# Kernel tuning notes

Hardware: AMD Instinct MI355X
Metric: run time of the kernel (lower is better)

Reference implementation:

```python
import jax, jax.numpy as jnp
import numpy as np

B, L, E, H, Dff = 2, 2048, 1024, 16, 4096
Dh = E // H


def _ln(x, g, b, eps=1e-5):
    m = jnp.mean(x, axis=-1, keepdims=True)
    v = jnp.mean((x - m) ** 2, axis=-1, keepdims=True)
    return (x - m) / jnp.sqrt(v + eps) * g + b


def setup_inputs() -> dict:
    key = jax.random.key(0)
    ks = jax.random.split(key, 16)
    s_e = 1.0 / np.sqrt(E)
    s_d = 1.0 / np.sqrt(Dff)
    inp = {
        "x": jax.random.normal(ks[0], (B, L, E), jnp.float32),
        # causal mask: positions with 0 are masked out (masked_fill(mask==0, -1e9))
        "mask": jnp.tril(jnp.ones((L, L), jnp.bool_)),
        # per-head QKV projections, stacked over heads: (H, E, Dh), biases (H, Dh)
        "Wq": jax.random.uniform(ks[1], (H, E, Dh), jnp.float32, -s_e, s_e),
        "bq": jax.random.uniform(ks[2], (H, Dh), jnp.float32, -s_e, s_e),
        "Wk": jax.random.uniform(ks[3], (H, E, Dh), jnp.float32, -s_e, s_e),
        "bk": jax.random.uniform(ks[4], (H, Dh), jnp.float32, -s_e, s_e),
        "Wv": jax.random.uniform(ks[5], (H, E, Dh), jnp.float32, -s_e, s_e),
        "bv": jax.random.uniform(ks[6], (H, Dh), jnp.float32, -s_e, s_e),
        "Wo": jax.random.uniform(ks[7], (E, E), jnp.float32, -s_e, s_e),
        "bo": jax.random.uniform(ks[8], (E,), jnp.float32, -s_e, s_e),
        "W1": jax.random.uniform(ks[9], (E, Dff), jnp.float32, -s_e, s_e),
        "c1": jax.random.uniform(ks[10], (Dff,), jnp.float32, -s_e, s_e),
        "W2": jax.random.uniform(ks[11], (Dff, E), jnp.float32, -s_d, s_d),
        "c2": jax.random.uniform(ks[12], (E,), jnp.float32, -s_d, s_d),
        "g1": jnp.ones((E,), jnp.float32),
        "beta1": jnp.zeros((E,), jnp.float32),
        "g2": jnp.ones((E,), jnp.float32),
        "beta2": jnp.zeros((E,), jnp.float32),
    }
    return inp


def reference(x, mask, Wq, bq, Wk, bk, Wv, bv, Wo, bo, W1, c1, W2, c2, g1, beta1, g2, beta2):
    # Batched equivalent of the per-head Attention loop (eval mode: dropout = identity)
    q = jnp.einsum("ble,hed->bhld", x, Wq) + bq[None, :, None, :]
    k = jnp.einsum("ble,hed->bhld", x, Wk) + bk[None, :, None, :]
    v = jnp.einsum("ble,hed->bhld", x, Wv) + bv[None, :, None, :]
    scores = jnp.einsum("bhld,bhmd->bhlm", q, k) / np.sqrt(Dh).astype(np.float32)
    scores = jnp.where(mask[None, None, :, :], scores, -1e9)
    p = jax.nn.softmax(scores, axis=-1)
    z = jnp.einsum("bhlm,bhmd->bhld", p, v)  # (B,H,L,Dh)
    z = z.transpose(0, 2, 1, 3).reshape(B, L, E)  # concat heads
    att = z @ Wo + bo
    h = _ln(x + att, g1, beta1)
    ff = jax.nn.relu(h @ W1 + c1) @ W2 + c2
    out = _ln(h + ff, g2, beta2)
    return out
```

## Files before the change

kernel.cpp:

```cpp
#include <hip/hip_runtime.h>
#include <hip/hip_bf16.h>
#include <math.h>

#define B_   2
#define L_   2048
#define E_   1024
#define H_   16
#define DH   64
#define DFF  4096
#define M_   4096
#define APAD 72
#define SCALE_Q 0.18033688011112042f

typedef __attribute__((ext_vector_type(8))) short short8;
typedef __attribute__((ext_vector_type(4))) float f32x4;
typedef __bf16 bf16x8 __attribute__((ext_vector_type(8)));

__device__ __forceinline__ float bf2f(unsigned short u) {
    return __uint_as_float(((unsigned)u) << 16);
}
__device__ __forceinline__ unsigned short f2bf(float f) {
    unsigned u = __float_as_uint(f);
    return (unsigned short)((u + 0x7fff + ((u >> 16) & 1)) >> 16);
}
__device__ __forceinline__ unsigned pk_trunc(float lo, float hi) {
    return (__float_as_uint(lo) >> 16) | (__float_as_uint(hi) & 0xffff0000u);
}

__device__ __forceinline__ void gld16(const unsigned short* g, unsigned short* l) {
    __builtin_amdgcn_global_load_lds(
        (const __attribute__((address_space(1))) void*)g,
        (__attribute__((address_space(3))) void*)l, 16, 0, 0);
}

__global__ __launch_bounds__(256) void prep(const float* __restrict__ x,
                                            const float* __restrict__ Wq,
                                            const float* __restrict__ Wk,
                                            const float* __restrict__ Wv,
                                            const float* __restrict__ bq,
                                            const float* __restrict__ bk,
                                            const float* __restrict__ bv,
                                            const float* __restrict__ Wo,
                                            const float* __restrict__ W1,
                                            const float* __restrict__ W2,
                                            unsigned short* __restrict__ xb,
                                            unsigned short* __restrict__ Wqkvt,
                                            unsigned short* __restrict__ Wot,
                                            unsigned short* __restrict__ W1t,
                                            unsigned short* __restrict__ W2t,
                                            float* __restrict__ bqkv) {
    __shared__ float tile[32][33];
    int bid = blockIdx.x;
    const int t = threadIdx.x;

    if (bid < 4096) {
        int i = (bid * 256 + t) * 4;
        float4 v = *(const float4*)&x[i];
        ushort4 pk = { f2bf(v.x), f2bf(v.y), f2bf(v.z), f2bf(v.w) };
        *(ushort4*)&xb[i] = pk;
        return;
    }
    bid -= 4096;

    const float* in; unsigned short* outp; int R, C, r0, c0; float sc = 1.f;
    if (bid < 3072) {
        int xq = bid & 1, yq = (bid >> 1) & 31, wh = bid >> 6;
        int which = wh >> 4, h = wh & 15;
        in   = (which == 0 ? Wq : which == 1 ? Wk : Wv) + (size_t)h * E_ * DH;
        outp = Wqkvt + ((size_t)which * 1024 + h * 64) * 1024;
        R = E_; C = DH; r0 = yq * 32; c0 = xq * 32;
        if (which == 0) sc = SCALE_Q;
    } else if (bid < 4096) {
        bid -= 3072;
        in = Wo; outp = Wot; R = E_; C = E_;
        c0 = (bid & 31) * 32; r0 = (bid >> 5) * 32;
    } else if (bid < 8192) {
        bid -= 4096;
        in = W1; outp = W1t; R = E_; C = DFF;
        c0 = (bid & 127) * 32; r0 = (bid >> 7) * 32;
    } else if (bid < 12288) {
        bid -= 8192;
        in = W2; outp = W2t; R = DFF; C = E_;
        c0 = (bid & 31) * 32; r0 = (bid >> 5) * 32;
    } else {
        bid -= 12288;
        int n = bid * 256 + t;
        bqkv[n] = n < 1024 ? bq[n] * SCALE_Q : n < 2048 ? bk[n - 1024] : bv[n - 2048];
        return;
    }

    const int tx = t & 31, tq = t >> 5;
#pragma unroll
    for (int s2 = 0; s2 < 4; s2++)
        tile[tq * 4 + s2][tx] = in[(size_t)(r0 + tq * 4 + s2) * C + c0 + tx] * sc;
    __syncthreads();
#pragma unroll
    for (int s2 = 0; s2 < 4; s2++)
        outp[(size_t)(c0 + tq * 4 + s2) * R + r0 + tx] = f2bf(tile[tx][tq * 4 + s2]);
}

__global__ __launch_bounds__(256) void v_transpose_perm(const unsigned short* __restrict__ qkv,
                                                        unsigned short* __restrict__ vtg) {
    __shared__ unsigned short tile[64 * APAD];
    const int t  = threadIdx.x;
    const int kt = blockIdx.x, hh = blockIdx.y, b = blockIdx.z;
    const int rr0 = t >> 3, o8 = (t & 7) * 8, rr1 = rr0 + 32;
    const size_t gbase = ((size_t)b * L_ + kt * 64) * 3072 + 2048 + hh * 64;
    *(short8*)&tile[rr0 * APAD + o8] = *(const short8*)&qkv[gbase + (size_t)rr0 * 3072 + o8];
    *(short8*)&tile[rr1 * APAD + o8] = *(const short8*)&qkv[gbase + (size_t)rr1 * 3072 + o8];
    __syncthreads();
    const size_t obase = ((size_t)(b * H_ + hh) * 64) * (size_t)L_ + kt * 64;
    const int a = t & 15, d0 = (t >> 4) * 4;
#pragma unroll
    for (int s2 = 0; s2 < 4; s2++) {
        int d = d0 + s2;
        ushort4 pk = { tile[(a +  0) * APAD + d], tile[(a + 16) * APAD + d],
                       tile[(a + 32) * APAD + d], tile[(a + 48) * APAD + d] };
        *(ushort4*)&vtg[obase + (size_t)d * L_ + 4 * a] = pk;
    }
}

#define BAR() __builtin_amdgcn_s_barrier()
#define LGKM0() do { asm volatile("s_waitcnt lgkmcnt(0)" ::: "memory"); \
                     __builtin_amdgcn_sched_barrier(0); } while (0)

#define G256_READ_A(qr) do {                                                  \
    _Pragma("unroll") for (int mi = 0; mi < 4; mi++)                          \
    _Pragma("unroll") for (int ks = 0; ks < 2; ks++)                          \
        afr[mi][ks] = *(const bf16x8*)&As[bb + ((qr) * 128 + aRow + mi * 16) * 64 + (ks ? cs1 : cs0)]; \
} while (0)

#define G256_READ_B(qc) do {                                                  \
    _Pragma("unroll") for (int nj = 0; nj < 2; nj++)                          \
    _Pragma("unroll") for (int ks = 0; ks < 2; ks++)                          \
        bfr[qc][nj][ks] = *(const bf16x8*)&Bs[bb + ((qc) * 128 + bRow + nj * 16) * 64 + (ks ? cs1 : cs0)]; \
} while (0)

#define G256_MFMA(qr, qc) do {                                                \
    __builtin_amdgcn_s_setprio(1);                                            \
    _Pragma("unroll") for (int mi = 0; mi < 4; mi++)                          \
    _Pragma("unroll") for (int nj = 0; nj < 2; nj++)                          \
    _Pragma("unroll") for (int ks = 0; ks < 2; ks++)                          \
        acc[qr][qc][mi][nj] = __builtin_amdgcn_mfma_f32_16x16x32_bf16(        \
            afr[mi][ks], bfr[qc][nj][ks], acc[qr][qc][mi][nj], 0, 0, 0);      \
    __builtin_amdgcn_s_setprio(0);                                            \
} while (0)

template <int RELU, int SK>
__global__ __launch_bounds__(512, 2) void gemm256(const unsigned short* __restrict__ A,
                                                  const unsigned short* __restrict__ Bt,
                                                  const float* __restrict__ bias,
                                                  unsigned short* __restrict__ P0,
                                                  unsigned short* __restrict__ P1,
                                                  unsigned short* __restrict__ P2,
                                                  unsigned short* __restrict__ P3,
                                                  int M, int N, int K) {
    extern __shared__ __align__(16) unsigned short g_lds[];
    unsigned short* As = g_lds;
    unsigned short* Bs = g_lds + 32768;

    const int t    = threadIdx.x;
    const int lane = t & 63;
    const int w    = t >> 6;
    const int quad = lane >> 4;
    const int l16  = lane & 15;

    const int lin = blockIdx.x;
    const int xcd = lin & 7, s = lin >> 3;
    int m0, n0, kbeg, KT;
    unsigned short* C;
    if (SK) {
        m0 = ((xcd << 1) | (s & 1)) * 256;
        const int rest = s >> 1;
        n0 = (rest & 3) * 256;
        const int z  = rest >> 2;
        const int K4 = K >> 2;
        kbeg = z * K4;
        KT   = K4 >> 6;
        C = (z == 0) ? P0 : (z == 1) ? P1 : (z == 2) ? P2 : P3;
    } else {
        const int NT2 = (N >> 8) >> 1;
        m0 = (((xcd & 3) << 2) | (s & 3)) * 256;
        n0 = ((xcd >> 2) * NT2 + (s >> 2)) * 256;
        kbeg = 0;
        KT   = K >> 6;
        C = P0;
    }

    const int srow = t >> 3;
    const int ksw  = ((t & 7) ^ (srow & 7)) * 8;
    const size_t aStage = (size_t)(m0 + srow) * K + kbeg + ksw;
    const size_t bStage = (size_t)(n0 + srow) * K + kbeg + ksw;

    auto stageA = [&](int buf, int h, int v) {
        size_t g = aStage + (size_t)(h * 128) * K + (size_t)v * 64;
        unsigned short* l = As + buf * 16384 + h * 8192 + w * 512;
        gld16(A + g, l);
        gld16(A + g + (size_t)64 * K, l + 4096);
    };
    auto stageB = [&](int buf, int h, int v) {
        size_t g = bStage + (size_t)(h * 128) * K + (size_t)v * 64;
        unsigned short* l = Bs + buf * 16384 + h * 8192 + w * 512;
        gld16(Bt + g, l);
        gld16(Bt + g + (size_t)64 * K, l + 4096);
    };

    const int aRow = (w >> 2) * 64 + l16;
    const int bRow = (w & 3) * 32 + l16;
    const int cs0  = (quad ^ (l16 & 7)) * 8;
    const int cs1  = cs0 ^ 32;

    f32x4 acc[2][2][4][2];
#pragma unroll
    for (int a1 = 0; a1 < 2; a1++)
#pragma unroll
        for (int a2 = 0; a2 < 2; a2++)
#pragma unroll
            for (int a3 = 0; a3 < 4; a3++)
#pragma unroll
                for (int a4 = 0; a4 < 2; a4++)
                    acc[a1][a2][a3][a4] = (f32x4){0.f, 0.f, 0.f, 0.f};

    bf16x8 afr[4][2], bfr[2][2][2];

    stageA(0, 0, 0); stageA(0, 1, 0); stageB(0, 0, 0); stageB(0, 1, 0);
    if (KT > 1) {
        stageA(1, 0, 1); stageB(1, 0, 1);
        asm volatile("s_waitcnt vmcnt(4)" ::: "memory");
    } else {
        asm volatile("s_waitcnt vmcnt(0)" ::: "memory");
    }
    BAR();

    for (int u = 0; u < KT; ++u) {
        const int bb = (u & 1) * 16384;
        const int nb = ((u + 1) & 1);

        G256_READ_A(0);
        G256_READ_B(0);
        if (u + 1 < KT) stageB(nb, 1, u + 1);
        BAR(); LGKM0();
        G256_MFMA(0, 0);
        BAR();

        G256_READ_B(1);
        if (u + 1 < KT) stageA(nb, 1, u + 1);
        BAR(); LGKM0();
        G256_MFMA(0, 1);
        BAR();

        G256_READ_A(1);
        if (u + 2 < KT) stageA(u & 1, 0, u + 2);
        BAR(); LGKM0();
        G256_MFMA(1, 0);
        BAR();

        if (u + 2 < KT) {
            stageB(u & 1, 0, u + 2);
            asm volatile("s_waitcnt vmcnt(4)" ::: "memory");
        } else {
            asm volatile("s_waitcnt vmcnt(0)" ::: "memory");
        }
        BAR(); LGKM0();
        G256_MFMA(1, 1);
        BAR();
    }

#pragma unroll
    for (int qr = 0; qr < 2; qr++)
#pragma unroll
        for (int qc = 0; qc < 2; qc++)
#pragma unroll
            for (int nj = 0; nj < 2; nj++) {
                const int col = n0 + qc * 128 + (w & 3) * 32 + nj * 16 + l16;
                const float bv = SK ? 0.f : bias[col];
#pragma unroll
                for (int mi = 0; mi < 4; mi++) {
                    const int row = m0 + qr * 128 + (w >> 2) * 64 + mi * 16 + quad * 4;
#pragma unroll
                    for (int r = 0; r < 4; r++) {
                        float v = acc[qr][qc][mi][nj][r] + bv;
                        if (RELU) v = fmaxf(v, 0.f);
                        C[(size_t)(row + r) * N + col] = f2bf(v);
                    }
                }
            }
}

__global__ __launch_bounds__(256, 2) void attn_mfma(const unsigned short* __restrict__ qkv,
                                                    const unsigned short* __restrict__ vtg,
                                                    unsigned short* __restrict__ oA,
                                                    unsigned short* __restrict__ oB,
                                                    float* __restrict__ lA,
                                                    float* __restrict__ lB) {
    __shared__ __align__(16) unsigned short ks[2][64 * APAD];
    __shared__ __align__(16) unsigned short vt[64 * APAD];
    __shared__ __align__(16) unsigned short ps[128 * APAD];

    const int t    = threadIdx.x;
    const int lane = t & 63;
    const int w    = t >> 6;
    const int l16  = lane & 15;
    const int quad = lane >> 4;

    const int lin  = blockIdx.x;
    const int unit = lin >> 8;
    const int l8   = lin & 255;
    const int xcd  = l8 & 7;
    const int s    = l8 >> 3;
    const int hh   = xcd * 2 + (s & 1);
    const int rest = s >> 1;
    const int b    = rest & 1;
    const int pair = rest >> 1;

    unsigned short* __restrict__ oP = unit ? oB : oA;
    float* __restrict__ lP = unit ? lB : lA;

    const size_t rowbase = (size_t)b * L_;
    const size_t vbase   = ((size_t)(b * H_ + hh) * 64) * (size_t)L_;
    const int rr0 = t >> 3, o8 = (t & 7) * 8, rr1 = rr0 + 32;

    for (int ph = 0; ph < 2; ph++) {
        const int qq = ph ? pair : 15 - pair;
        const int cnt = qq + 1;

        bf16x8 qf[2][2];
#pragma unroll
        for (int g = 0; g < 2; g++) {
            size_t qrow = rowbase + qq * 128 + w * 32 + g * 16 + l16;
#pragma unroll
            for (int c = 0; c < 2; c++)
                qf[g][c] = *(const bf16x8*)&qkv[qrow * 3072 + hh * 64 + c * 32 + quad * 8];
        }

        f32x4 o[2][4];
#pragma unroll
        for (int g = 0; g < 2; g++)
#pragma unroll
            for (int j = 0; j < 4; j++) o[g][j] = (f32x4){0.f, 0.f, 0.f, 0.f};
        float l_i[2][4] = {};

        {
            size_t kg = (rowbase + unit * 64) * 3072 + 1024 + hh * 64;
            short8 k0 = *(const short8*)&qkv[kg + (size_t)rr0 * 3072 + o8];
            short8 k1 = *(const short8*)&qkv[kg + (size_t)rr1 * 3072 + o8];
            short8 v0 = *(const short8*)&vtg[vbase + unit * 64 + (size_t)rr0 * L_ + o8];
            short8 v1 = *(const short8*)&vtg[vbase + unit * 64 + (size_t)rr1 * L_ + o8];
            *(short8*)&ks[0][rr0 * APAD + o8] = k0;
            *(short8*)&ks[0][rr1 * APAD + o8] = k1;
            *(short8*)&vt[rr0 * APAD + o8] = v0;
            *(short8*)&vt[rr1 * APAD + o8] = v1;
        }

        short8 kr0, kr1, vr0, vr1;
        for (int i = 0; i < cnt; i++) {
            const int kt = unit + 2 * i;
            const int p  = i & 1;
            __syncthreads();

            if (i + 1 < cnt) {
                size_t kg = (rowbase + (kt + 2) * 64) * 3072 + 1024 + hh * 64;
                kr0 = *(const short8*)&qkv[kg + (size_t)rr0 * 3072 + o8];
                kr1 = *(const short8*)&qkv[kg + (size_t)rr1 * 3072 + o8];
                size_t vg = vbase + (kt + 2) * 64;
                vr0 = *(const short8*)&vtg[vg + (size_t)rr0 * L_ + o8];
                vr1 = *(const short8*)&vtg[vg + (size_t)rr1 * L_ + o8];
            }

            f32x4 s4[2][4];
#pragma unroll
            for (int g = 0; g < 2; g++)
#pragma unroll
                for (int j = 0; j < 4; j++) s4[g][j] = (f32x4){0.f, 0.f, 0.f, 0.f};
            __builtin_amdgcn_s_setprio(1);
#pragma unroll
            for (int c = 0; c < 2; c++)
#pragma unroll
                for (int j = 0; j < 4; j++) {
                    bf16x8 kf = *(const bf16x8*)&ks[p][(j * 16 + l16) * APAD + c * 32 + quad * 8];
#pragma unroll
                    for (int g = 0; g < 2; g++)
                        s4[g][j] = __builtin_amdgcn_mfma_f32_16x16x32_bf16(qf[g][c], kf, s4[g][j], 0, 0, 0);
                }
            __builtin_amdgcn_s_setprio(0);

            if (kt >= 2 * qq) {
#pragma unroll
                for (int g = 0; g < 2; g++)
#pragma unroll
                    for (int j = 0; j < 4; j++) {
                        int lk = kt * 64 + j * 16 + l16;
#pragma unroll
                        for (int r = 0; r < 4; r++)
                            if (lk > qq * 128 + w * 32 + g * 16 + quad * 4 + r)
                                s4[g][j][r] = -INFINITY;
                    }
            }

#pragma unroll
            for (int g = 0; g < 2; g++)
#pragma unroll
                for (int r = 0; r < 4; r++) {
                    float p0 = __builtin_amdgcn_exp2f(s4[g][0][r]);
                    float p1 = __builtin_amdgcn_exp2f(s4[g][1][r]);
                    float p2 = __builtin_amdgcn_exp2f(s4[g][2][r]);
                    float p3 = __builtin_amdgcn_exp2f(s4[g][3][r]);
                    l_i[g][r] += (p0 + p1) + (p2 + p3);
                    uint2 pk = { pk_trunc(p0, p1), pk_trunc(p2, p3) };
                    *(uint2*)&ps[(w * 32 + g * 16 + quad * 4 + r) * APAD + 4 * l16] = pk;
                }

            __builtin_amdgcn_s_waitcnt(0xc07f);

            __builtin_amdgcn_s_setprio(1);
#pragma unroll
            for (int c = 0; c < 2; c++) {
                bf16x8 pf[2];
#pragma unroll
                for (int g = 0; g < 2; g++)
                    pf[g] = *(const bf16x8*)&ps[(w * 32 + g * 16 + l16) * APAD + c * 32 + quad * 8];
#pragma unroll
                for (int j = 0; j < 4; j++) {
                    bf16x8 vf = *(const bf16x8*)&vt[(j * 16 + l16) * APAD + c * 32 + quad * 8];
#pragma unroll
                    for (int g = 0; g < 2; g++)
                        o[g][j] = __builtin_amdgcn_mfma_f32_16x16x32_bf16(pf[g], vf, o[g][j], 0, 0, 0);
                }
            }
            __builtin_amdgcn_s_setprio(0);

            __syncthreads();
            if (i + 1 < cnt) {
                *(short8*)&ks[p ^ 1][rr0 * APAD + o8] = kr0;
                *(short8*)&ks[p ^ 1][rr1 * APAD + o8] = kr1;
                *(short8*)&vt[rr0 * APAD + o8] = vr0;
                *(short8*)&vt[rr1 * APAD + o8] = vr1;
            }
        }

#pragma unroll
        for (int g = 0; g < 2; g++)
#pragma unroll
            for (int r = 0; r < 4; r++) {
                float l = l_i[g][r];
                l += __shfl_xor(l, 1);
                l += __shfl_xor(l, 2);
                l += __shfl_xor(l, 4);
                l += __shfl_xor(l, 8);
                int rowq = qq * 128 + w * 32 + g * 16 + quad * 4 + r;
                size_t grow = (size_t)(b * H_ + hh) * L_ + rowq;
                if (l16 == 0) lP[grow] = l;
#pragma unroll
                for (int j = 0; j < 4; j++)
                    oP[grow * 64 + j * 16 + l16] = f2bf(o[g][j][r]);
            }
    }
}

__global__ __launch_bounds__(256) void attn_combine(const unsigned short* __restrict__ oA,
                                                    const unsigned short* __restrict__ oB,
                                                    const float* __restrict__ lA,
                                                    const float* __restrict__ lB,
                                                    unsigned short* __restrict__ zb) {
    const int t = threadIdx.x;
    const size_t idx4 = ((size_t)blockIdx.x * 256 + t) * 4;
    const size_t row  = idx4 >> 6;
    const int    col  = (int)(idx4 & 63);

    float inv = 1.f / (lA[row] + lB[row]);
    ushort4 ua = *(const ushort4*)&oA[idx4];
    ushort4 ub = *(const ushort4*)&oB[idx4];

    const int bq   = (int)(row >> 15);
    const int hh   = (int)((row >> 11) & 15);
    const int rowq = (int)(row & 2047);
    size_t z = ((size_t)(bq * L_ + rowq)) * 1024 + hh * 64 + col;
    ushort4 pk = { f2bf((bf2f(ua.x) + bf2f(ub.x)) * inv),
                   f2bf((bf2f(ua.y) + bf2f(ub.y)) * inv),
                   f2bf((bf2f(ua.z) + bf2f(ub.z)) * inv),
                   f2bf((bf2f(ua.w) + bf2f(ub.w)) * inv) };
    *(ushort4*)&zb[z] = pk;
}

template <int WRITE_BF16>
__global__ __launch_bounds__(256) void ln5_kernel(const float* __restrict__ a,
                                                  const unsigned short* __restrict__ q0,
                                                  const unsigned short* __restrict__ q1,
                                                  const unsigned short* __restrict__ q2,
                                                  const unsigned short* __restrict__ q3,
                                                  const float* __restrict__ bias,
                                                  const float* __restrict__ g,
                                                  const float* __restrict__ be,
                                                  float* __restrict__ out,
                                                  unsigned short* __restrict__ out_bf) {
    __shared__ float s1[256], s2[256];
    const int row = blockIdx.x;
    const int t   = threadIdx.x;
    const size_t base = (size_t)row * E_ + t * 4;

    float4 ya = *(const float4*)&a[base];
    ushort4 u0 = *(const ushort4*)&q0[base];
    ushort4 u1 = *(const ushort4*)&q1[base];
    ushort4 u2 = *(const ushort4*)&q2[base];
    ushort4 u3 = *(const ushort4*)&q3[base];
    float4 bb = *(const float4*)&bias[t * 4];
    float y0 = ya.x + bb.x + bf2f(u0.x) + bf2f(u1.x) + bf2f(u2.x) + bf2f(u3.x);
    float y1 = ya.y + bb.y + bf2f(u0.y) + bf2f(u1.y) + bf2f(u2.y) + bf2f(u3.y);
    float y2 = ya.z + bb.z + bf2f(u0.z) + bf2f(u1.z) + bf2f(u2.z) + bf2f(u3.z);
    float y3 = ya.w + bb.w + bf2f(u0.w) + bf2f(u1.w) + bf2f(u2.w) + bf2f(u3.w);

    s1[t] = y0 + y1 + y2 + y3;
    s2[t] = y0 * y0 + y1 * y1 + y2 * y2 + y3 * y3;
    __syncthreads();
    for (int off = 128; off > 0; off >>= 1) {
        if (t < off) { s1[t] += s1[t + off]; s2[t] += s2[t + off]; }
        __syncthreads();
    }
    float mean = s1[0] * (1.0f / E_);
    float var  = s2[0] * (1.0f / E_) - mean * mean;
    float rstd = rsqrtf(var + 1e-5f);

    float4 gv = *(const float4*)&g[t * 4];
    float4 bv = *(const float4*)&be[t * 4];
    float4 ov;
    ov.x = (y0 - mean) * rstd * gv.x + bv.x;
    ov.y = (y1 - mean) * rstd * gv.y + bv.y;
    ov.z = (y2 - mean) * rstd * gv.z + bv.z;
    ov.w = (y3 - mean) * rstd * gv.w + bv.w;
    *(float4*)&out[base] = ov;
    if (WRITE_BF16) {
        ushort4 pk = { f2bf(ov.x), f2bf(ov.y), f2bf(ov.z), f2bf(ov.w) };
        *(ushort4*)&out_bf[base] = pk;
    }
}

extern "C" void kernel_launch(void* const* d_in, const int* in_sizes, int n_in,
                              void* d_out, int out_size, void* d_ws, size_t ws_size,
                              hipStream_t stream)
{
    const float* x     = (const float*)d_in[0];
    const float* Wq    = (const float*)d_in[2];
    const float* bq    = (const float*)d_in[3];
    const float* Wk    = (const float*)d_in[4];
    const float* bk    = (const float*)d_in[5];
    const float* Wv    = (const float*)d_in[6];
    const float* bv    = (const float*)d_in[7];
    const float* Wo    = (const float*)d_in[8];
    const float* bo    = (const float*)d_in[9];
    const float* W1    = (const float*)d_in[10];
    const float* c1    = (const float*)d_in[11];
    const float* W2    = (const float*)d_in[12];
    const float* c2    = (const float*)d_in[13];
    const float* g1    = (const float*)d_in[14];
    const float* beta1 = (const float*)d_in[15];
    const float* g2    = (const float*)d_in[16];
    const float* beta2 = (const float*)d_in[17];
    float* out = (float*)d_out;

    const size_t MB = 1024 * 1024;
    char* w = (char*)d_ws;
    unsigned short* xb    = (unsigned short*)(w + 0 * MB);
    unsigned short* Wqkvt = (unsigned short*)(w + 8 * MB);
    unsigned short* Wot   = (unsigned short*)(w + 14 * MB);
    unsigned short* W1t   = (unsigned short*)(w + 16 * MB);
    unsigned short* W2t   = (unsigned short*)(w + 24 * MB);
    float*          bqkv  = (float*)(w + 32 * MB);
    unsigned short* qkv   = (unsigned short*)(w + 33 * MB);
    float*          h     = (float*)(w + 65 * MB);
    unsigned short* vtg   = (unsigned short*)(w + 89 * MB);
    unsigned short* oPA   = (unsigned short*)(w + 57 * MB);
    unsigned short* oPB   = (unsigned short*)(w + 81 * MB);
    float*          lPA   = (float*)(w + 32 * MB);
    float*          lPB   = (float*)(w + 32 * MB + 262144);
    unsigned short* zb    = (unsigned short*)(w + 0 * MB);
    unsigned short* ap0   = (unsigned short*)(w + 33 * MB);
    unsigned short* ap1   = (unsigned short*)(w + 41 * MB);
    unsigned short* ap2   = (unsigned short*)(w + 49 * MB);
    unsigned short* ap3   = (unsigned short*)(w + 89 * MB);
    unsigned short* hb    = (unsigned short*)(w + 0 * MB);
    unsigned short* ff1b  = (unsigned short*)(w + 33 * MB);
    unsigned short* fp0   = (unsigned short*)(w + 0 * MB);
    unsigned short* fp1   = (unsigned short*)(w + 8 * MB);
    unsigned short* fp2   = (unsigned short*)(w + 16 * MB);
    unsigned short* fp3   = (unsigned short*)(w + 81 * MB);

    static bool lds_inited = false;
    if (!lds_inited) {
        (void)hipFuncSetAttribute((const void*)&gemm256<0, 0>,
                                  hipFuncAttributeMaxDynamicSharedMemorySize, 131072);
        (void)hipFuncSetAttribute((const void*)&gemm256<1, 0>,
                                  hipFuncAttributeMaxDynamicSharedMemorySize, 131072);
        (void)hipFuncSetAttribute((const void*)&gemm256<0, 1>,
                                  hipFuncAttributeMaxDynamicSharedMemorySize, 131072);
        lds_inited = true;
    }

    dim3 blk(256);
    dim3 blk2(512);

    prep<<<dim3(16396), blk, 0, stream>>>(x, Wq, Wk, Wv, bq, bk, bv, Wo, W1, W2,
                                          xb, Wqkvt, Wot, W1t, W2t, bqkv);

    gemm256<0, 0><<<dim3(192), blk2, 131072, stream>>>(xb, Wqkvt, bqkv,
                                                       qkv, nullptr, nullptr, nullptr,
                                                       M_, 3072, E_);

    v_transpose_perm<<<dim3(L_ / 64, H_, B_), blk, 0, stream>>>(qkv, vtg);

    attn_mfma<<<dim3(512), blk, 0, stream>>>(qkv, vtg, oPA, oPB, lPA, lPB);

    attn_combine<<<dim3(4096), blk, 0, stream>>>(oPA, oPB, lPA, lPB, zb);

    gemm256<0, 1><<<dim3(256), blk2, 131072, stream>>>(zb, Wot, nullptr,
                                                       ap0, ap1, ap2, ap3,
                                                       M_, E_, E_);

    ln5_kernel<1><<<dim3(M_), blk, 0, stream>>>(x, ap0, ap1, ap2, ap3, bo, g1, beta1, h, hb);

    gemm256<1, 0><<<dim3(256), blk2, 131072, stream>>>(hb, W1t, c1,
                                                       ff1b, nullptr, nullptr, nullptr,
                                                       M_, DFF, E_);

    gemm256<0, 1><<<dim3(256), blk2, 131072, stream>>>(ff1b, W2t, nullptr,
                                                       fp0, fp1, fp2, fp3,
                                                       M_, E_, DFF);

    ln5_kernel<0><<<dim3(M_), blk, 0, stream>>>(h, fp0, fp1, fp2, fp3, c2, g2, beta2, out, nullptr);
}
```

Before: 331.6 us.

## Double-buffer LDS fragment registers and prefetch next tile during MFMA

Replaces the single set of A/B register fragments in the 256x256 GEMM main loop with two ping-pong sets. The next k-step's first A/B fragments are now read from LDS while the last MFMA quadrant runs, and the explicit lgkmcnt(0) waits plus sched_barriers are removed so the compiler can overlap LDS reads with MFMAs. The aim is to hide LDS latency behind matrix work. In exchange it uses more VGPRs under launch_bounds(512,2) and leaves wait placement to compiler-inserted waitcnts.

```diff
diff --git a/kernel.cpp b/kernel.cpp
--- a/kernel.cpp
+++ b/kernel.cpp
@@ -121,28 +121,26 @@
 }
 
 #define BAR() __builtin_amdgcn_s_barrier()
-#define LGKM0() do { asm volatile("s_waitcnt lgkmcnt(0)" ::: "memory"); \
-                     __builtin_amdgcn_sched_barrier(0); } while (0)
-
-#define G256_READ_A(qr) do {                                                  \
+
+#define RD_A(DST, BB, QR) do {                                                \
     _Pragma("unroll") for (int mi = 0; mi < 4; mi++)                          \
     _Pragma("unroll") for (int ks = 0; ks < 2; ks++)                          \
-        afr[mi][ks] = *(const bf16x8*)&As[bb + ((qr) * 128 + aRow + mi * 16) * 64 + (ks ? cs1 : cs0)]; \
+        DST[mi][ks] = *(const bf16x8*)&As[(BB) * 16384 + ((QR) * 128 + aRow + mi * 16) * 64 + (ks ? cs1 : cs0)]; \
 } while (0)
 
-#define G256_READ_B(qc) do {                                                  \
+#define RD_B(DST, BB, QC) do {                                                \
     _Pragma("unroll") for (int nj = 0; nj < 2; nj++)                          \
     _Pragma("unroll") for (int ks = 0; ks < 2; ks++)                          \
-        bfr[qc][nj][ks] = *(const bf16x8*)&Bs[bb + ((qc) * 128 + bRow + nj * 16) * 64 + (ks ? cs1 : cs0)]; \
+        DST[nj][ks] = *(const bf16x8*)&Bs[(BB) * 16384 + ((QC) * 128 + bRow + nj * 16) * 64 + (ks ? cs1 : cs0)]; \
 } while (0)
 
-#define G256_MFMA(qr, qc) do {                                                \
+#define MM(QR, QC, AF, BF) do {                                               \
     __builtin_amdgcn_s_setprio(1);                                            \
     _Pragma("unroll") for (int mi = 0; mi < 4; mi++)                          \
     _Pragma("unroll") for (int nj = 0; nj < 2; nj++)                          \
     _Pragma("unroll") for (int ks = 0; ks < 2; ks++)                          \
-        acc[qr][qc][mi][nj] = __builtin_amdgcn_mfma_f32_16x16x32_bf16(        \
-            afr[mi][ks], bfr[qc][nj][ks], acc[qr][qc][mi][nj], 0, 0, 0);      \
+        acc[QR][QC][mi][nj] = __builtin_amdgcn_mfma_f32_16x16x32_bf16(        \
+            AF[mi][ks], BF[nj][ks], acc[QR][QC][mi][nj], 0, 0, 0);            \
     __builtin_amdgcn_s_setprio(0);                                            \
 } while (0)
 
@@ -212,18 +210,18 @@
 
     f32x4 acc[2][2][4][2];
 #pragma unroll
-    for (int a1 = 0; a1 < 2; a1++)
+    for (int a1i = 0; a1i < 2; a1i++)
 #pragma unroll
         for (int a2 = 0; a2 < 2; a2++)
 #pragma unroll
             for (int a3 = 0; a3 < 4; a3++)
 #pragma unroll
                 for (int a4 = 0; a4 < 2; a4++)
-                    acc[a1][a2][a3][a4] = (f32x4){0.f, 0.f, 0.f, 0.f};
-
-    bf16x8 afr[4][2], bfr[2][2][2];
-
-    stageA(0, 0, 0); stageA(0, 1, 0); stageB(0, 0, 0); stageB(0, 1, 0);
+                    acc[a1i][a2][a3][a4] = (f32x4){0.f, 0.f, 0.f, 0.f};
+
+    bf16x8 a0[4][2], a1[4][2], b0[2][2], b1[2][2];
+
+    stageA(0, 0, 0); stageB(0, 0, 0); stageA(0, 1, 0); stageB(0, 1, 0);
     if (KT > 1) {
         stageA(1, 0, 1); stageB(1, 0, 1);
         asm volatile("s_waitcnt vmcnt(4)" ::: "memory");
@@ -231,38 +229,42 @@
         asm volatile("s_waitcnt vmcnt(0)" ::: "memory");
     }
     BAR();
+    RD_A(a0, 0, 0);
+    RD_B(b0, 0, 0);
 
     for (int u = 0; u < KT; ++u) {
-        const int bb = (u & 1) * 16384;
-        const int nb = ((u + 1) & 1);
-
-        G256_READ_A(0);
-        G256_READ_B(0);
+        const int bb = u & 1;
+        const int nb = bb ^ 1;
+
+        RD_B(b1, bb, 1);
         if (u + 1 < KT) stageB(nb, 1, u + 1);
-        BAR(); LGKM0();
-        G256_MFMA(0, 0);
-        BAR();
-
-        G256_READ_B(1);
+        BAR();
+        MM(0, 0, a0, b0);
+        BAR();
+
+        RD_A(a1, bb, 1);
         if (u + 1 < KT) stageA(nb, 1, u + 1);
-        BAR(); LGKM0();
-        G256_MFMA(0, 1);
-        BAR();
-
-        G256_READ_A(1);
-        if (u + 2 < KT) stageA(u & 1, 0, u + 2);
-        BAR(); LGKM0();
-        G256_MFMA(1, 0);
+        BAR();
+        MM(0, 1, a0, b1);
+        BAR();
+
+        if (u + 2 < KT) stageA(bb, 0, u + 2);
+        BAR();
+        MM(1, 0, a1, b0);
         BAR();
 
         if (u + 2 < KT) {
-            stageB(u & 1, 0, u + 2);
+            stageB(bb, 0, u + 2);
             asm volatile("s_waitcnt vmcnt(4)" ::: "memory");
-        } else {
+        } else if (u + 1 < KT) {
             asm volatile("s_waitcnt vmcnt(0)" ::: "memory");
         }
-        BAR(); LGKM0();
-        G256_MFMA(1, 1);
+        BAR();
+        if (u + 1 < KT) {
+            RD_A(a0, nb, 0);
+            RD_B(b0, nb, 0);
+        }
+        MM(1, 1, a1, b1);
         BAR();
     }
 
```

After: 335.4 us. About the same (+1.1%).
